# Optimization experiments

Measured on AMD Instinct MI355X. Metric: run time of the kernel, lower is better.

## Reference

```python
import jax, jax.numpy as jnp
import numpy as np

B, N, D, H = 4, 4096, 1024, 16
DH = D // H              # 64
M = int(DH * np.log(DH))  # 266 random features (performer-pytorch default)
EPS = 1e-4


def softmax_kernel(t, proj, is_query):
    # t: [B,H,N,DH], proj: [M,DH]  -> [B,H,N,M]  (FAVOR+ positive features)
    dn = t.shape[-1] ** -0.25
    ratio = proj.shape[0] ** -0.5
    td = jnp.einsum('bhnd,md->bhnm', t * dn, proj)
    diag = 0.5 * (dn ** 2) * jnp.sum(t * t, axis=-1, keepdims=True)  # [B,H,N,1]
    if is_query:
        mx = jnp.max(td, axis=-1, keepdims=True)
    else:
        mx = jnp.max(td, axis=(-1, -2), keepdims=True)
    return ratio * (jnp.exp(td - diag - mx) + EPS)


def setup_inputs() -> dict:
    key = jax.random.key(0)
    ks = jax.random.split(key, 12)
    s = 0.02
    inp = {
        'x':   jax.random.normal(ks[0], (B, N, D), jnp.float32),
        'Wq':  jax.random.normal(ks[1], (D, D), jnp.float32) * s,
        'bq':  jnp.zeros((D,), jnp.float32),
        'Wk':  jax.random.normal(ks[2], (D, D), jnp.float32) * s,
        'bk':  jnp.zeros((D,), jnp.float32),
        'Wv':  jax.random.normal(ks[3], (D, D), jnp.float32) * s,
        'bv':  jnp.zeros((D,), jnp.float32),
        'Wo':  jax.random.normal(ks[4], (D, D), jnp.float32) * s,
        'bo':  jnp.zeros((D,), jnp.float32),
        'Wfc': jax.random.normal(ks[5], (D, D), jnp.float32) * s,
        'bfc': jnp.zeros((D,), jnp.float32),
        'proj': jax.random.normal(ks[6], (M, DH), jnp.float32),  # random feature projection (frozen)
    }
    return inp


def reference(x, Wq, bq, Wk, bk, Wv, bv, Wo, bo, Wfc, bfc, proj):
    b, n, d = x.shape
    def heads(t):  # [B,N,D] -> [B,H,N,DH]
        return t.reshape(b, n, H, DH).transpose(0, 2, 1, 3)
    q = heads(x @ Wq.T + bq)
    k = heads(x @ Wk.T + bk)
    v = heads(x @ Wv.T + bv)

    qp = softmax_kernel(q, proj, is_query=True)    # [B,H,N,M]
    kp = softmax_kernel(k, proj, is_query=False)   # [B,H,N,M]

    # non-causal linear attention: O(N*M*DH)
    k_sum = jnp.sum(kp, axis=-2)                               # [B,H,M]
    d_inv = 1.0 / jnp.einsum('bhnm,bhm->bhn', qp, k_sum)       # [B,H,N]
    context = jnp.einsum('bhnm,bhnd->bhmd', kp, v)             # [B,H,M,DH]
    out = jnp.einsum('bhmd,bhnm,bhn->bhnd', context, qp, d_inv)

    out = out.transpose(0, 2, 1, 3).reshape(b, n, d)           # merge heads
    h = out @ Wo.T + bo                                        # performer internal to_out
    return jax.nn.relu(h @ Wfc.T + bfc)                        # wrapper fc_out + ReLU
```

## Files before the change

### kernel.cpp

```cpp
#include <hip/hip_runtime.h>
#include <math.h>

#define B_ 4
#define N_ 4096
#define D_ 1024
#define H_ 16
#define DH_ 64
#define M_ 266
#define MP_ 320

#define DN_ 0.35355339059327373f
#define RATIO_ 0.06131393394849658f
#define EPS_ 1e-4f
#define KP_ 72
#define NSPLIT_ 16
#define PARTSZ_ ((size_t)64 * M_ * 64)

typedef __attribute__((ext_vector_type(8))) short bfrag;
typedef __attribute__((ext_vector_type(4))) float f4;

__device__ __forceinline__ unsigned f2ord(float f) {
    unsigned u = __float_as_uint(f);
    return (u & 0x80000000u) ? ~u : (u | 0x80000000u);
}
// ... 7 lines not shown
    if (i < n) p[i] = 0.f;
}

__device__ __forceinline__ void split2pack(float x, float y, unsigned* hp, unsigned* lp) {
    unsigned ux = __float_as_uint(x), uy = __float_as_uint(y);
    float hx = __uint_as_float(ux & 0xffff0000u);
    float hy = __uint_as_float(uy & 0xffff0000u);
    float lx = x - hx, ly = y - hy;
    *hp = (ux >> 16) | (uy & 0xffff0000u);
    *lp = (__float_as_uint(lx) >> 16) | (__float_as_uint(ly) & 0xffff0000u);
}
__device__ __forceinline__ unsigned short bf16rne(float x) {
    unsigned u = __float_as_uint(x);
    return (unsigned short)((u + 0x7fffu + ((u >> 16) & 1u)) >> 16);
}

__device__ __forceinline__ void async_cp16(const void* g, void* l) {
    __builtin_amdgcn_global_load_lds(
        (const __attribute__((address_space(1))) void*)g,
        (__attribute__((address_space(3))) void*)l, 16, 0, 0);
}

__global__ __launch_bounds__(256) void split_f32(const float* __restrict__ X,
        unsigned short* __restrict__ Xh, unsigned short* __restrict__ Xl, int n4)
{
    int i = blockIdx.x * 256 + threadIdx.x;
    if (i >= n4) return;
    const float4 v = ((const float4*)X)[i];
    unsigned h0, l0, h1, l1;
    split2pack(v.x, v.y, &h0, &l0);
    split2pack(v.z, v.w, &h1, &l1);
    ((uint2*)Xh)[i] = make_uint2(h0, h1);
    ((uint2*)Xl)[i] = make_uint2(l0, l1);
}

__global__ __launch_bounds__(256) void split_w5(const float* __restrict__ W0,
        const float* __restrict__ W1, const float* __restrict__ W2,
        const float* __restrict__ W3, const float* __restrict__ W4,
        unsigned short* __restrict__ Wsp)
{
    int sel = blockIdx.y;
    const float* W = (sel == 0) ? W0 : (sel == 1) ? W1 : (sel == 2) ? W2 : (sel == 3) ? W3 : W4;
    unsigned short* h = Wsp + (size_t)sel * 2097152;
    unsigned short* l = h + 1048576;
    int i = blockIdx.x * 256 + threadIdx.x;
    const float4 v = ((const float4*)W)[i];
    unsigned h0, l0, h1, l1;
    split2pack(v.x, v.y, &h0, &l0);
    split2pack(v.z, v.w, &h1, &l1);
    ((uint2*)h)[i] = make_uint2(h0, h1);
    ((uint2*)l)[i] = make_uint2(l0, l1);
}

__global__ __launch_bounds__(256) void gemm_qkv_s(
        const unsigned short* __restrict__ Ah, const unsigned short* __restrict__ Al,
        const unsigned short* __restrict__ Wsp,
        const float* __restrict__ b0, const float* __restrict__ b1, const float* __restrict__ b2,
        float* __restrict__ C0, float* __restrict__ C1, float* __restrict__ C2)
{
    __shared__ __align__(16) unsigned short Ahs[128 * 32];
    __shared__ __align__(16) unsigned short Als[128 * 32];
    __shared__ __align__(16) unsigned short Bhs[128 * 32];
    __shared__ __align__(16) unsigned short Bls[128 * 32];

    int tid = threadIdx.x;
    int flat = blockIdx.y * 24 + blockIdx.x;
    int newid = (flat & 7) * 384 + (flat >> 3);
    int bm = (newid / 24) * 128;
    int rmod = newid % 24;
    int sel = rmod >> 3;
    int bn = (rmod & 7) * 128;
    const unsigned short* Bh = Wsp + (size_t)sel * 2097152;
    const unsigned short* Bl = Bh + 1048576;
    const float* bias = (sel == 0) ? b0 : (sel == 1) ? b1 : b2;
    float* C = (sel == 0) ? C0 : (sel == 1) ? C1 : C2;

    int lane = tid & 63;
    int w = tid >> 6;
    int wm = w >> 1, wn = w & 1;
    int ml = lane & 15, kq = lane >> 4;
    int rsub = lane >> 2;
    int ksw = (((lane & 3) ^ ((lane >> 3) & 3))) * 8;
    int slot8 = ((kq ^ ((ml >> 1) & 3))) * 8;

    f4 acc[4][4];
    #pragma unroll
    for (int i = 0; i < 4; ++i)
        #pragma unroll
        for (int j = 0; j < 4; ++j)
            acc[i][j] = (f4){0.f, 0.f, 0.f, 0.f};

    for (int kt = 0; kt < D_; kt += 32) {
        __syncthreads();
        #pragma unroll
        for (int j = 0; j < 2; ++j) {
            int row = w * 32 + j * 16;
            size_t ga = (size_t)(bm + row + rsub) * D_ + kt + ksw;
            size_t gb = (size_t)(bn + row + rsub) * D_ + kt + ksw;
            async_cp16(Ah + ga, &Ahs[row * 32]);
            async_cp16(Al + ga, &Als[row * 32]);
            async_cp16(Bh + gb, &Bhs[row * 32]);
            async_cp16(Bl + gb, &Bls[row * 32]);
        }
        __syncthreads();
        bfrag ah[4], al[4], bh[4], bl[4];
        #pragma unroll
        for (int i = 0; i < 4; ++i) {
            int arow = wm * 64 + i * 16 + ml;
            ah[i] = *(const bfrag*)&Ahs[arow * 32 + slot8];
            al[i] = *(const bfrag*)&Als[arow * 32 + slot8];
            int brow = wn * 64 + i * 16 + ml;
            bh[i] = *(const bfrag*)&Bhs[brow * 32 + slot8];
            bl[i] = *(const bfrag*)&Bls[brow * 32 + slot8];
        }
        #pragma unroll
        for (int mi = 0; mi < 4; ++mi)
            #pragma unroll
            for (int ni = 0; ni < 4; ++ni) {
                acc[mi][ni] = __builtin_amdgcn_mfma_f32_16x16x32_bf16(ah[mi], bh[ni], acc[mi][ni], 0, 0, 0);
                acc[mi][ni] = __builtin_amdgcn_mfma_f32_16x16x32_bf16(al[mi], bh[ni], acc[mi][ni], 0, 0, 0);
                acc[mi][ni] = __builtin_amdgcn_mfma_f32_16x16x32_bf16(ah[mi], bl[ni], acc[mi][ni], 0, 0, 0);
            }
    }
    #pragma unroll
    for (int ni = 0; ni < 4; ++ni) {
        int col = bn + wn * 64 + ni * 16 + ml;
        float bv = bias[col];
        #pragma unroll
        for (int mi = 0; mi < 4; ++mi) {
            int row0 = bm + wm * 64 + mi * 16 + kq * 4;
            #pragma unroll
            for (int r = 0; r < 4; ++r)
                C[(size_t)(row0 + r) * D_ + col] = acc[mi][ni][r] + bv;
        }
    }
}

__global__ __launch_bounds__(256) void gemm_nt_s(
        const unsigned short* __restrict__ Ah, const unsigned short* __restrict__ Al,
        const unsigned short* __restrict__ Bh, const unsigned short* __restrict__ Bl,
        const float* __restrict__ bias, float* __restrict__ C,
        unsigned short* __restrict__ Ch, unsigned short* __restrict__ Cl, int mode)
{
    __shared__ __align__(16) unsigned short Ahs[128 * 32];
    __shared__ __align__(16) unsigned short Als[128 * 32];
    __shared__ __align__(16) unsigned short Bhs[128 * 32];
    __shared__ __align__(16) unsigned short Bls[128 * 32];

    int tid = threadIdx.x;
    int flat = blockIdx.y * 8 + blockIdx.x;
    int newid = (flat & 7) * 128 + (flat >> 3);
    int bm = (newid >> 3) * 128;
    int bn = (newid & 7) * 128;
    int lane = tid & 63;
    int w = tid >> 6;
    int wm = w >> 1, wn = w & 1;
    int ml = lane & 15, kq = lane >> 4;
    int rsub = lane >> 2;
    int ksw = (((lane & 3) ^ ((lane >> 3) & 3))) * 8;
    int slot8 = ((kq ^ ((ml >> 1) & 3))) * 8;

    f4 acc[4][4];
    #pragma unroll
    for (int i = 0; i < 4; ++i)
        #pragma unroll
        for (int j = 0; j < 4; ++j)
            acc[i][j] = (f4){0.f, 0.f, 0.f, 0.f};

    for (int kt = 0; kt < D_; kt += 32) {
        __syncthreads();
        #pragma unroll
        for (int j = 0; j < 2; ++j) {
            int row = w * 32 + j * 16;
            size_t ga = (size_t)(bm + row + rsub) * D_ + kt + ksw;
            size_t gb = (size_t)(bn + row + rsub) * D_ + kt + ksw;
            async_cp16(Ah + ga, &Ahs[row * 32]);
            async_cp16(Al + ga, &Als[row * 32]);
            async_cp16(Bh + gb, &Bhs[row * 32]);
            async_cp16(Bl + gb, &Bls[row * 32]);
        }
        __syncthreads();
        bfrag ah[4], al[4], bh[4], bl[4];
        #pragma unroll
        for (int i = 0; i < 4; ++i) {
            int arow = wm * 64 + i * 16 + ml;
            ah[i] = *(const bfrag*)&Ahs[arow * 32 + slot8];
            al[i] = *(const bfrag*)&Als[arow * 32 + slot8];
            int brow = wn * 64 + i * 16 + ml;
            bh[i] = *(const bfrag*)&Bhs[brow * 32 + slot8];
            bl[i] = *(const bfrag*)&Bls[brow * 32 + slot8];
        }
        #pragma unroll
        for (int mi = 0; mi < 4; ++mi)
            #pragma unroll
            for (int ni = 0; ni < 4; ++ni) {
                acc[mi][ni] = __builtin_amdgcn_mfma_f32_16x16x32_bf16(ah[mi], bh[ni], acc[mi][ni], 0, 0, 0);
                acc[mi][ni] = __builtin_amdgcn_mfma_f32_16x16x32_bf16(al[mi], bh[ni], acc[mi][ni], 0, 0, 0);
                acc[mi][ni] = __builtin_amdgcn_mfma_f32_16x16x32_bf16(ah[mi], bl[ni], acc[mi][ni], 0, 0, 0);
            }
    }
    #pragma unroll
    for (int ni = 0; ni < 4; ++ni) {
        int col = bn + wn * 64 + ni * 16 + ml;
        float bv = bias[col];
        #pragma unroll
        for (int mi = 0; mi < 4; ++mi) {
            int row0 = bm + wm * 64 + mi * 16 + kq * 4;
            #pragma unroll
            for (int r = 0; r < 4; ++r) {
                float o = acc[mi][ni][r] + bv;
                size_t idx = (size_t)(row0 + r) * D_ + col;
                if (mode == 2) {
                    unsigned u = __float_as_uint(o);
                    float lo = o - __uint_as_float(u & 0xffff0000u);
                    Ch[idx] = (unsigned short)(u >> 16);
                    Cl[idx] = (unsigned short)(__float_as_uint(lo) >> 16);
                } else {
                    if (mode == 1) o = fmaxf(o, 0.f);
                    C[idx] = o;
                }
            }
        }
    }
}

__global__ __launch_bounds__(256) void kside(
    const float* __restrict__ Kin, const float* __restrict__ Vin,
    const float* __restrict__ proj,
    float* __restrict__ S_u, float* __restrict__ Cpart, float* __restrict__ C_u,
    float* __restrict__ Vsum, unsigned int* __restrict__ mxp)
{
    __shared__ __align__(16) unsigned short Kh[64 * KP_];
    __shared__ __align__(16) unsigned short VT[64 * KP_];
    __shared__ __align__(16) unsigned short Ph[2][64 * KP_];
    __shared__ __align__(16) unsigned short Us[64 * KP_];
    __shared__ __align__(16) float Ssum[MP_];
    __shared__ float diag[64];
    float* redf = (float*)Us;

    int bh = blockIdx.y, b = bh >> 4, h = bh & 15;
    int s = blockIdx.x;
    int n0 = s * 256;
    int tid = threadIdx.x, lane = tid & 63, w = tid >> 6;
    int ml = lane & 15, quad = lane >> 4;

    float* dstC = (s < NSPLIT_ - 1) ? (Cpart + (size_t)s * PARTSZ_) : C_u;

    for (int i = tid; i < MP_; i += 256) Ssum[i] = 0.f;

    f4 acc[5][4];
    #pragma unroll
    for (int i = 0; i < 5; ++i)
        #pragma unroll
        for (int j = 0; j < 4; ++j) acc[i][j] = (f4){0.f, 0.f, 0.f, 0.f};
    float vs[4] = {0.f, 0.f, 0.f, 0.f};
    float lmax = -1e30f;

    for (int nc = 0; nc < 4; ++nc) {
        __syncthreads();
        #pragma unroll
        for (int l = 0; l < 4; ++l) {
            int idx = tid + 256 * l;
            int r = idx >> 4;
            int d4 = (idx & 15) * 4;
            size_t g = ((size_t)(b * N_ + n0 + nc * 64 + r)) * D_ + h * DH_ + d4;
            const float4 kv = *(const float4*)(Kin + g);
            redf[r * 17 + (tid & 15)] = kv.x * kv.x + kv.y * kv.y + kv.z * kv.z + kv.w * kv.w;
            unsigned w0 = (unsigned)bf16rne(kv.x * DN_) | ((unsigned)bf16rne(kv.y * DN_) << 16);
            unsigned w1 = (unsigned)bf16rne(kv.z * DN_) | ((unsigned)bf16rne(kv.w * DN_) << 16);
            *(uint2*)&Kh[r * KP_ + d4] = make_uint2(w0, w1);
            const float4 vv = *(const float4*)(Vin + g);
            vs[0] += vv.x; vs[1] += vv.y; vs[2] += vv.z; vs[3] += vv.w;
            VT[(d4 + 0) * KP_ + r] = bf16rne(vv.x);
            VT[(d4 + 1) * KP_ + r] = bf16rne(vv.y);
            VT[(d4 + 2) * KP_ + r] = bf16rne(vv.z);
            VT[(d4 + 3) * KP_ + r] = bf16rne(vv.w);
        }
        {
            #pragma unroll
            for (int l = 0; l < 2; ++l) {
                int idx = tid + 256 * l;
                int m = idx >> 3, d8 = (idx & 7) * 8;
                const float4 p0 = *(const float4*)(proj + m * 64 + d8);
                const float4 p1 = *(const float4*)(proj + m * 64 + d8 + 4);
                unsigned a0 = (unsigned)bf16rne(p0.x) | ((unsigned)bf16rne(p0.y) << 16);
                unsigned a1 = (unsigned)bf16rne(p0.z) | ((unsigned)bf16rne(p0.w) << 16);
                unsigned a2 = (unsigned)bf16rne(p1.x) | ((unsigned)bf16rne(p1.y) << 16);
                unsigned a3 = (unsigned)bf16rne(p1.z) | ((unsigned)bf16rne(p1.w) << 16);
                *(uint4*)&Ph[0][m * KP_ + d8] = make_uint4(a0, a1, a2, a3);
            }
        }
        __syncthreads();
        if (tid < 64) {
            float ss = 0.f;
            #pragma unroll
            for (int p = 0; p < 16; ++p) ss += redf[tid * 17 + p];
            diag[tid] = ss * 0.0625f;
        }
        __syncthreads();

        bfrag kh0 = *(const bfrag*)&Kh[(w * 16 + ml) * KP_ + quad * 8];
        bfrag kh1 = *(const bfrag*)&Kh[(w * 16 + ml) * KP_ + 32 + quad * 8];
        float dgv[4];
        #pragma unroll
        for (int r = 0; r < 4; ++r) dgv[r] = diag[w * 16 + quad * 4 + r];

        for (int mc = 0; mc < 5; ++mc) {
            int pb = mc & 1;
            float4 pf[4];
            if (mc < 4) {
                #pragma unroll
                for (int l = 0; l < 2; ++l) {
                    int idx = tid + 256 * l;
                    int m = idx >> 3, d8 = (idx & 7) * 8;
                    int mg = (mc + 1) * 64 + m;
                    if (mg < M_) {
                        pf[l * 2 + 0] = *(const float4*)(proj + mg * 64 + d8);
                        pf[l * 2 + 1] = *(const float4*)(proj + mg * 64 + d8 + 4);
                    } else {
                        pf[l * 2 + 0] = make_float4(0.f, 0.f, 0.f, 0.f);
                        pf[l * 2 + 1] = make_float4(0.f, 0.f, 0.f, 0.f);
                    }
                }
            }
            #pragma unroll
            for (int mt = 0; mt < 4; ++mt) {
                int mrow = mt * 16 + ml;
                bfrag ph0 = *(const bfrag*)&Ph[pb][mrow * KP_ + quad * 8];
                bfrag ph1 = *(const bfrag*)&Ph[pb][mrow * KP_ + 32 + quad * 8];
                f4 t = (f4){0.f, 0.f, 0.f, 0.f};
                t = __builtin_amdgcn_mfma_f32_16x16x32_bf16(kh0, ph0, t, 0, 0, 0);
                t = __builtin_amdgcn_mfma_f32_16x16x32_bf16(kh1, ph1, t, 0, 0, 0);
                bool mv = (mc * 64 + mrow) < M_;
                float su = 0.f;
                unsigned short up[4];
                #pragma unroll
                for (int r = 0; r < 4; ++r) {
                    float u = 0.f;
                    if (mv) {
                        float tt = t[r];
                        lmax = fmaxf(lmax, tt);
                        u = __expf(tt - dgv[r]);
                    }
                    su += u;
                    up[r] = bf16rne(u);
                }
                su += __shfl_xor(su, 16);
                su += __shfl_xor(su, 32);
                if (mv && quad == 0) atomicAdd(&Ssum[mc * 64 + mrow], su);
                unsigned w0 = (unsigned)up[0] | ((unsigned)up[1] << 16);
                unsigned w1 = (unsigned)up[2] | ((unsigned)up[3] << 16);
                *(uint2*)&Us[mrow * KP_ + w * 16 + quad * 4] = make_uint2(w0, w1);
            }
            if (mc < 4) {
                #pragma unroll
                for (int l = 0; l < 2; ++l) {
                    int idx = tid + 256 * l;
                    int m = idx >> 3, d8 = (idx & 7) * 8;
                    const float4 p0 = pf[l * 2 + 0], p1 = pf[l * 2 + 1];
                    unsigned a0 = (unsigned)bf16rne(p0.x) | ((unsigned)bf16rne(p0.y) << 16);
                    unsigned a1 = (unsigned)bf16rne(p0.z) | ((unsigned)bf16rne(p0.w) << 16);
                    unsigned a2 = (unsigned)bf16rne(p1.x) | ((unsigned)bf16rne(p1.y) << 16);
                    unsigned a3 = (unsigned)bf16rne(p1.z) | ((unsigned)bf16rne(p1.w) << 16);
                    *(uint4*)&Ph[1 - pb][m * KP_ + d8] = make_uint4(a0, a1, a2, a3);
                }
            }
            __syncthreads();
            bfrag ua0 = *(const bfrag*)&Us[(w * 16 + ml) * KP_ + quad * 8];
            bfrag ua1 = *(const bfrag*)&Us[(w * 16 + ml) * KP_ + 32 + quad * 8];
            #pragma unroll
            for (int dt = 0; dt < 4; ++dt) {
                bfrag vb0 = *(const bfrag*)&VT[(dt * 16 + ml) * KP_ + quad * 8];
                bfrag vb1 = *(const bfrag*)&VT[(dt * 16 + ml) * KP_ + 32 + quad * 8];
                acc[mc][dt] = __builtin_amdgcn_mfma_f32_16x16x32_bf16(ua0, vb0, acc[mc][dt], 0, 0, 0);
                acc[mc][dt] = __builtin_amdgcn_mfma_f32_16x16x32_bf16(ua1, vb1, acc[mc][dt], 0, 0, 0);
            }
            __syncthreads();
        }
    }
    #pragma unroll
    for (int mc = 0; mc < 5; ++mc)
        #pragma unroll
        for (int dt = 0; dt < 4; ++dt)
            #pragma unroll
            for (int r = 0; r < 4; ++r) {
                int m = mc * 64 + w * 16 + quad * 4 + r;
                if (m < M_)
                    dstC[((size_t)bh * M_ + m) * 64 + dt * 16 + ml] = acc[mc][dt][r];
            }
    __syncthreads();
    for (int m = tid; m < M_; m += 256)
        atomicAdd(S_u + bh * M_ + m, Ssum[m]);
    #pragma unroll
    for (int off = 32; off; off >>= 1) lmax = fmaxf(lmax, __shfl_xor(lmax, off));
    __syncthreads();
    if (lane == 0) redf[w] = lmax;
    __syncthreads();
    if (tid == 0) {
        float mxv = fmaxf(fmaxf(redf[0], redf[1]), fmaxf(redf[2], redf[3]));
        atomicMax(mxp + bh, f2ord(mxv));
    }
    for (int j = 0; j < 4; ++j) {
        __syncthreads();
        redf[tid] = vs[j];
        __syncthreads();
        if (tid < 16) {
            float ss = 0.f;
            #pragma unroll
            for (int p = 0; p < 16; ++p) ss += redf[tid + 16 * p];
            atomicAdd(Vsum + bh * 64 + tid * 4 + j, ss);
        }
    }
}

__global__ __launch_bounds__(256) void finalize_kernel(
    const float* __restrict__ S_u, const float* __restrict__ Cpart, const float* __restrict__ C_u,
    const float* __restrict__ Vsum, const unsigned* __restrict__ mxp,
// ... 7 lines not shown
    float emx = __expf(-ord2f(mxp[bh]));

    float csacc = 0.f;
    #pragma unroll
    for (int i = 0; i < 16; ++i) {
        int idx = i * 256 + tid;
        int dh = idx & 63, mloc = idx >> 6;
        int m = mc * 64 + mloc;
        float v = 0.f;
        if (m < M_) {
            size_t off = ((size_t)bh * M_ + m) * 64 + dh;
            float sacc = C_u[off];
            for (int sp = 0; sp < NSPLIT_ - 1; ++sp)
                sacc += Cpart[(size_t)sp * PARTSZ_ + off];
            v = RATIO_ * (emx * sacc + EPS_ * Vsum[bh * 64 + dh]);
        }
        T[mloc * 65 + dh] = v;
        csacc += v;
    }
    red[tid] = csacc;
    __syncthreads();
    if (tid < 64) atomicAdd(&Cs[bh * 64 + tid], red[tid] + red[tid + 64] + red[tid + 128] + red[tid + 192]);
    float ksl = 0.f;
    if (tid < 64) {
        int m = mc * 64 + tid;
        float kv = (m < M_) ? RATIO_ * (emx * S_u[bh * M_ + m] + EPS_ * (float)N_) : 0.f;
        ksum_f[bh * MP_ + m] = kv;
        ksl = kv;
    }
    __syncthreads();
    red[tid] = ksl;
    __syncthreads();
    if (tid == 0) {
        float ss = 0.f;
        for (int p = 0; p < 64; ++p) ss += red[p];
        atomicAdd(kss + bh, ss);
    }
    __syncthreads();
    #pragma unroll
    for (int i = 0; i < 8; ++i) {
        int idx = i * 256 + tid;
        int dh = idx >> 5, m2 = (idx & 31) * 2;
        float v0 = T[m2 * 65 + dh], v1 = T[(m2 + 1) * 65 + dh];
        unsigned u0 = __float_as_uint(v0), u1 = __float_as_uint(v1);
        float lo0 = v0 - __uint_as_float(u0 & 0xffff0000u);
        float lo1 = v1 - __uint_as_float(u1 & 0xffff0000u);
        size_t dst = ((size_t)(bh * 64 + dh)) * MP_ + mc * 64 + m2;
        *(unsigned*)&ctxTh[dst] = (u0 >> 16) | (u1 & 0xffff0000u);
        *(unsigned*)&ctxTl[dst] = (__float_as_uint(lo0) >> 16) | (__float_as_uint(lo1) & 0xffff0000u);
    }
}

__global__ __launch_bounds__(256) void qattn(
    const float* __restrict__ Q, const float* __restrict__ proj,
    const float* __restrict__ ksum_f, const unsigned short* __restrict__ ctxTh,
    const unsigned short* __restrict__ ctxTl,
    const float* __restrict__ Cs, const float* __restrict__ kss,
    unsigned short* __restrict__ attnH, unsigned short* __restrict__ attnL)
{
    __shared__ __align__(16) unsigned short Qh[64 * KP_], Ql[64 * KP_];
    __shared__ __align__(16) unsigned short Ph[64 * KP_], Pl[64 * KP_];
    __shared__ __align__(16) unsigned short Uh[64 * KP_], Ul[64 * KP_];
    __shared__ __align__(16) float ks[MP_];
    __shared__ float diag[64];
    float* redf = (float*)Uh;

    int bh = blockIdx.y, b = bh >> 4, h = bh & 15;
    int n0 = blockIdx.x * 64;
    int tid = threadIdx.x, lane = tid & 63, w = tid >> 6;
    int ml = lane & 15, quad = lane >> 4;

    #pragma unroll
    for (int l = 0; l < 4; ++l) {
        int idx = tid + 256 * l;
        int r = idx >> 4, d4 = (idx & 15) * 4;
        size_t g = ((size_t)(b * N_ + n0 + r)) * D_ + h * DH_ + d4;
        const float4 qv = *(const float4*)(Q + g);
        redf[r * 17 + (tid & 15)] = qv.x * qv.x + qv.y * qv.y + qv.z * qv.z + qv.w * qv.w;
        unsigned h0, l0, h1, l1;
        split2pack(qv.x * DN_, qv.y * DN_, &h0, &l0);
        split2pack(qv.z * DN_, qv.w * DN_, &h1, &l1);
        *(uint2*)&Qh[r * KP_ + d4] = make_uint2(h0, h1);
        *(uint2*)&Ql[r * KP_ + d4] = make_uint2(l0, l1);
    }
    for (int m = tid; m < MP_; m += 256) ks[m] = ksum_f[bh * MP_ + m];
    __syncthreads();
    if (tid < 64) {
        float s = 0.f;
        #pragma unroll
        for (int p = 0; p < 16; ++p) s += redf[tid * 17 + p];
        diag[tid] = s * 0.0625f;
    }
    __syncthreads();

    bfrag qh0 = *(const bfrag*)&Qh[(w * 16 + ml) * KP_ + quad * 8];
    bfrag ql0 = *(const bfrag*)&Ql[(w * 16 + ml) * KP_ + quad * 8];
    bfrag qh1 = *(const bfrag*)&Qh[(w * 16 + ml) * KP_ + 32 + quad * 8];
    bfrag ql1 = *(const bfrag*)&Ql[(w * 16 + ml) * KP_ + 32 + quad * 8];
    float dg = diag[w * 16 + ml];
    float dacc = 0.f, tmax = -1e30f;
    f4 oacc[4];
    #pragma unroll
    for (int i = 0; i < 4; ++i) oacc[i] = (f4){0.f, 0.f, 0.f, 0.f};

    for (int mc = 0; mc < 5; ++mc) {
        #pragma unroll
        for (int l = 0; l < 4; ++l) {
            int idx = tid + 256 * l;
            int m = idx >> 4, d4 = (idx & 15) * 4;
            int mg = mc * 64 + m;
            float4 p = make_float4(0.f, 0.f, 0.f, 0.f);
            if (mg < M_) p = *(const float4*)(proj + mg * 64 + d4);
            unsigned h0, l0, h1, l1;
            split2pack(p.x, p.y, &h0, &l0);
            split2pack(p.z, p.w, &h1, &l1);
            *(uint2*)&Ph[m * KP_ + d4] = make_uint2(h0, h1);
            *(uint2*)&Pl[m * KP_ + d4] = make_uint2(l0, l1);
        }
        __syncthreads();
        #pragma unroll
        for (int mt = 0; mt < 4; ++mt) {
            int mrow = mt * 16 + ml;
            bfrag ph0 = *(const bfrag*)&Ph[mrow * KP_ + quad * 8];
            bfrag pl0 = *(const bfrag*)&Pl[mrow * KP_ + quad * 8];
            bfrag ph1 = *(const bfrag*)&Ph[mrow * KP_ + 32 + quad * 8];
            bfrag pl1 = *(const bfrag*)&Pl[mrow * KP_ + 32 + quad * 8];
            f4 t = (f4){0.f, 0.f, 0.f, 0.f};
            t = __builtin_amdgcn_mfma_f32_16x16x32_bf16(ph0, qh0, t, 0, 0, 0);
            t = __builtin_amdgcn_mfma_f32_16x16x32_bf16(pl0, qh0, t, 0, 0, 0);
            t = __builtin_amdgcn_mfma_f32_16x16x32_bf16(ph0, ql0, t, 0, 0, 0);
            t = __builtin_amdgcn_mfma_f32_16x16x32_bf16(ph1, qh1, t, 0, 0, 0);
            t = __builtin_amdgcn_mfma_f32_16x16x32_bf16(pl1, qh1, t, 0, 0, 0);
            t = __builtin_amdgcn_mfma_f32_16x16x32_bf16(ph1, ql1, t, 0, 0, 0);
            const float4 ksv = *(const float4*)&ks[mc * 64 + mt * 16 + quad * 4];
            float ksa[4] = {ksv.x, ksv.y, ksv.z, ksv.w};
            unsigned short uh4[4], ul4[4];
            #pragma unroll
            for (int r = 0; r < 4; ++r) {
                int mg = mc * 64 + mt * 16 + quad * 4 + r;
                float tt = t[r];
                float u = __expf(tt - dg);
                if (mg < M_) tmax = fmaxf(tmax, tt);
                dacc = fmaf(u, ksa[r], dacc);
                unsigned uu = __float_as_uint(u);
                float lo = u - __uint_as_float(uu & 0xffff0000u);
                uh4[r] = (unsigned short)(uu >> 16);
                ul4[r] = (unsigned short)(__float_as_uint(lo) >> 16);
            }
            unsigned a0 = (unsigned)uh4[0] | ((unsigned)uh4[1] << 16);
            unsigned a1 = (unsigned)uh4[2] | ((unsigned)uh4[3] << 16);
            unsigned b0 = (unsigned)ul4[0] | ((unsigned)ul4[1] << 16);
            unsigned b1 = (unsigned)ul4[2] | ((unsigned)ul4[3] << 16);
            *(uint2*)&Uh[(w * 16 + ml) * KP_ + mt * 16 + quad * 4] = make_uint2(a0, a1);
            *(uint2*)&Ul[(w * 16 + ml) * KP_ + mt * 16 + quad * 4] = make_uint2(b0, b1);
        }
        __syncthreads();
        #pragma unroll
        for (int l = 0; l < 2; ++l) {
            int idx = tid + 256 * l;
            int dh = idx >> 3, m8 = (idx & 7) * 8;
            size_t src = ((size_t)(bh * 64 + dh)) * MP_ + mc * 64 + m8;
            *(uint4*)&Ph[dh * KP_ + m8] = *(const uint4*)(ctxTh + src);
            *(uint4*)&Pl[dh * KP_ + m8] = *(const uint4*)(ctxTl + src);
        }
        __syncthreads();
        bfrag ua0h = *(const bfrag*)&Uh[(w * 16 + ml) * KP_ + quad * 8];
        bfrag ua0l = *(const bfrag*)&Ul[(w * 16 + ml) * KP_ + quad * 8];
        bfrag ua1h = *(const bfrag*)&Uh[(w * 16 + ml) * KP_ + 32 + quad * 8];
        bfrag ua1l = *(const bfrag*)&Ul[(w * 16 + ml) * KP_ + 32 + quad * 8];
        #pragma unroll
// ... 25 lines not shown
            float dv = __shfl(dinv, srcl);
            float fv = __shfl(fac, srcl);
            float o = (oacc[dt][r] + fv * csv) * dv;
            int n = n0 + w * 16 + quad * 4 + r;
            size_t gi = ((size_t)(b * N_ + n)) * D_ + h * DH_ + dt * 16 + ml;
            unsigned u = __float_as_uint(o);
            float lo = o - __uint_as_float(u & 0xffff0000u);
            attnH[gi] = (unsigned short)(u >> 16);
            attnL[gi] = (unsigned short)(__float_as_uint(lo) >> 16);
        }
    }
}

extern "C" void kernel_launch(void* const* d_in, const int* in_sizes, int n_in,
                              void* d_out, int out_size, void* d_ws, size_t ws_size,
                              hipStream_t stream)
{
    const float* x    = (const float*)d_in[0];
    const float* Wq   = (const float*)d_in[1];
    const float* bq   = (const float*)d_in[2];
    const float* Wk   = (const float*)d_in[3];
    const float* bk   = (const float*)d_in[4];
    const float* Wv   = (const float*)d_in[5];
    const float* bv   = (const float*)d_in[6];
    const float* Wo   = (const float*)d_in[7];
    const float* bo   = (const float*)d_in[8];
    const float* Wfc  = (const float*)d_in[9];
    const float* bfc  = (const float*)d_in[10];
    const float* proj = (const float*)d_in[11];
    float* out = (float*)d_out;

    float* ws = (float*)d_ws;
    const size_t nTok = (size_t)B_ * N_ * D_;
    const size_t nSu  = 64 * M_;
    const size_t nCu  = (size_t)64 * M_ * 64;
    const size_t nVs  = 64 * 64;
    const size_t nMx  = 64;
    const size_t nKsf = 64 * MP_;
    const size_t nCtx = (size_t)64 * MP_ * 64;
    const size_t nCs  = 64 * 64;

    const size_t offQ   = 0;
    const size_t offK   = nTok;
    const size_t offV   = nTok * 2;
    const size_t offSu  = nTok * 3;
    const size_t offCu  = offSu + nSu;
    const size_t offVs  = offCu + nCu;
    const size_t offMx  = offVs + nVs;
    const size_t offKsf = offMx + nMx;
    const size_t offCtx = offKsf + nKsf;
    const size_t offCs  = offCtx + nCtx;
    const size_t offKss = offCs + nCs;
    const size_t offWsp = offKss + 64;

    float* Q    = ws + offQ;
    float* Kb   = ws + offK;
    float* Vb   = ws + offV;
    float* S_u  = ws + offSu;
    float* C_u  = ws + offCu;
    float* Vsum = ws + offVs;
    unsigned* mx = (unsigned*)(ws + offMx);
    float* ksf  = ws + offKsf;
    unsigned short* ctxTh = (unsigned short*)(ws + offCtx);
    unsigned short* ctxTl = ctxTh + (size_t)64 * 64 * MP_;
    float* Cs   = ws + offCs;
    float* kss  = ws + offKss;
    unsigned short* Wsp = (unsigned short*)(ws + offWsp);

    unsigned short* xh = (unsigned short*)out;
    unsigned short* xl = xh + nTok;
    unsigned short* attnH = (unsigned short*)Kb;
    unsigned short* attnL = attnH + nTok;
    unsigned short* hbH = (unsigned short*)Vb;
    unsigned short* hbL = hbH + nTok;
    float* Cpart = out;

    int nzero = (int)(nSu + nCu + nVs + nMx + nKsf + nCtx + nCs + 64);
    zero_kernel<<<dim3((nzero + 255) / 256), dim3(256), 0, stream>>>(S_u, nzero);

    split_f32<<<dim3(16384), dim3(256), 0, stream>>>(x, xh, xl, (int)(nTok / 4));
    split_w5<<<dim3(1024, 5), dim3(256), 0, stream>>>(Wq, Wk, Wv, Wo, Wfc, Wsp);

    gemm_qkv_s<<<dim3(24, (B_ * N_) / 128), dim3(256), 0, stream>>>(
        xh, xl, Wsp, bq, bk, bv, Q, Kb, Vb);

    kside<<<dim3(NSPLIT_, 64), dim3(256), 0, stream>>>(Kb, Vb, proj, S_u, Cpart, C_u, Vsum, mx);
    finalize_kernel<<<dim3(5, 64), dim3(256), 0, stream>>>(S_u, Cpart, C_u, Vsum, mx, ksf, ctxTh, ctxTl, Cs, kss);
    qattn<<<dim3(64, 64), dim3(256), 0, stream>>>(Q, proj, ksf, ctxTh, ctxTl, Cs, kss, attnH, attnL);

    dim3 gg(D_ / 128, (B_ * N_) / 128);
    gemm_nt_s<<<gg, dim3(256), 0, stream>>>(attnH, attnL,
        Wsp + (size_t)3 * 2097152, Wsp + (size_t)3 * 2097152 + 1048576,
        bo, (float*)nullptr, hbH, hbL, 2);
    gemm_nt_s<<<gg, dim3(256), 0, stream>>>(hbH, hbL,
        Wsp + (size_t)4 * 2097152, Wsp + (size_t)4 * 2097152 + 1048576,
        bfc, out, (unsigned short*)nullptr, (unsigned short*)nullptr, 1);
}
```

Measured before the change: 988.7 us.

## Double-buffer LDS tiles in split-bf16 GEMMs and drop block swizzle

Both GEMM kernels now use two shared-memory buffers per operand and prefetch the next K tile while computing the current one, with one barrier per iteration instead of two. The intent is to overlap global-to-LDS async copies with MFMA work. The XCD-aware block-index remapping is removed in favour of plain grid indexing. Shared memory per block doubles to 64 KB, which can lower occupancy. The async copies have no explicit wait before the barrier, so it is unclear whether the prefetched data is guaranteed visible before it is read.

```diff
diff --git a/kernel.cpp b/kernel.cpp
--- a/kernel.cpp
+++ b/kernel.cpp
@@ -89,18 +89,15 @@
         const float* __restrict__ b0, const float* __restrict__ b1, const float* __restrict__ b2,
         float* __restrict__ C0, float* __restrict__ C1, float* __restrict__ C2)
 {
-    __shared__ __align__(16) unsigned short Ahs[128 * 32];
-    __shared__ __align__(16) unsigned short Als[128 * 32];
-    __shared__ __align__(16) unsigned short Bhs[128 * 32];
-    __shared__ __align__(16) unsigned short Bls[128 * 32];
+    __shared__ __align__(16) unsigned short Ahs[2][128 * 32];
+    __shared__ __align__(16) unsigned short Als[2][128 * 32];
+    __shared__ __align__(16) unsigned short Bhs[2][128 * 32];
+    __shared__ __align__(16) unsigned short Bls[2][128 * 32];
 
     int tid = threadIdx.x;
-    int flat = blockIdx.y * 24 + blockIdx.x;
-    int newid = (flat & 7) * 384 + (flat >> 3);
-    int bm = (newid / 24) * 128;
-    int rmod = newid % 24;
-    int sel = rmod >> 3;
-    int bn = (rmod & 7) * 128;
+    int sel = blockIdx.x >> 3;
+    int bn = (blockIdx.x & 7) * 128;
+    int bm = blockIdx.y * 128;
     const unsigned short* Bh = Wsp + (size_t)sel * 2097152;
     const unsigned short* Bl = Bh + 1048576;
     const float* bias = (sel == 0) ? b0 : (sel == 1) ? b1 : b2;
@@ -121,28 +118,34 @@
         for (int j = 0; j < 4; ++j)
             acc[i][j] = (f4){0.f, 0.f, 0.f, 0.f};
 
-    for (int kt = 0; kt < D_; kt += 32) {
-        __syncthreads();
+    auto STAGE = [&](int kt, int pb) {
         #pragma unroll
         for (int j = 0; j < 2; ++j) {
             int row = w * 32 + j * 16;
             size_t ga = (size_t)(bm + row + rsub) * D_ + kt + ksw;
             size_t gb = (size_t)(bn + row + rsub) * D_ + kt + ksw;
-            async_cp16(Ah + ga, &Ahs[row * 32]);
-            async_cp16(Al + ga, &Als[row * 32]);
-            async_cp16(Bh + gb, &Bhs[row * 32]);
-            async_cp16(Bl + gb, &Bls[row * 32]);
-        }
-        __syncthreads();
+            async_cp16(Ah + ga, &Ahs[pb][row * 32]);
+            async_cp16(Al + ga, &Als[pb][row * 32]);
+            async_cp16(Bh + gb, &Bhs[pb][row * 32]);
+            async_cp16(Bl + gb, &Bls[pb][row * 32]);
+        }
+    };
+
+    STAGE(0, 0);
+    __syncthreads();
+
+    for (int t = 0; t < 32; ++t) {
+        int pb = t & 1;
+        if (t < 31) STAGE((t + 1) * 32, pb ^ 1);
         bfrag ah[4], al[4], bh[4], bl[4];
         #pragma unroll
         for (int i = 0; i < 4; ++i) {
             int arow = wm * 64 + i * 16 + ml;
-            ah[i] = *(const bfrag*)&Ahs[arow * 32 + slot8];
-            al[i] = *(const bfrag*)&Als[arow * 32 + slot8];
+            ah[i] = *(const bfrag*)&Ahs[pb][arow * 32 + slot8];
+            al[i] = *(const bfrag*)&Als[pb][arow * 32 + slot8];
             int brow = wn * 64 + i * 16 + ml;
-            bh[i] = *(const bfrag*)&Bhs[brow * 32 + slot8];
-            bl[i] = *(const bfrag*)&Bls[brow * 32 + slot8];
+            bh[i] = *(const bfrag*)&Bhs[pb][brow * 32 + slot8];
+            bl[i] = *(const bfrag*)&Bls[pb][brow * 32 + slot8];
         }
         #pragma unroll
         for (int mi = 0; mi < 4; ++mi)
@@ -152,6 +155,7 @@
                 acc[mi][ni] = __builtin_amdgcn_mfma_f32_16x16x32_bf16(al[mi], bh[ni], acc[mi][ni], 0, 0, 0);
                 acc[mi][ni] = __builtin_amdgcn_mfma_f32_16x16x32_bf16(ah[mi], bl[ni], acc[mi][ni], 0, 0, 0);
             }
+        __syncthreads();
     }
     #pragma unroll
     for (int ni = 0; ni < 4; ++ni) {
@@ -173,16 +177,14 @@
         const float* __restrict__ bias, float* __restrict__ C,
         unsigned short* __restrict__ Ch, unsigned short* __restrict__ Cl, int mode)
 {
-    __shared__ __align__(16) unsigned short Ahs[128 * 32];
-    __shared__ __align__(16) unsigned short Als[128 * 32];
-    __shared__ __align__(16) unsigned short Bhs[128 * 32];
-    __shared__ __align__(16) unsigned short Bls[128 * 32];
+    __shared__ __align__(16) unsigned short Ahs[2][128 * 32];
+    __shared__ __align__(16) unsigned short Als[2][128 * 32];
+    __shared__ __align__(16) unsigned short Bhs[2][128 * 32];
+    __shared__ __align__(16) unsigned short Bls[2][128 * 32];
 
     int tid = threadIdx.x;
-    int flat = blockIdx.y * 8 + blockIdx.x;
-    int newid = (flat & 7) * 128 + (flat >> 3);
-    int bm = (newid >> 3) * 128;
-    int bn = (newid & 7) * 128;
+    int bn = blockIdx.x * 128;
+    int bm = blockIdx.y * 128;
     int lane = tid & 63;
     int w = tid >> 6;
     int wm = w >> 1, wn = w & 1;
@@ -198,28 +200,34 @@
         for (int j = 0; j < 4; ++j)
             acc[i][j] = (f4){0.f, 0.f, 0.f, 0.f};
 
-    for (int kt = 0; kt < D_; kt += 32) {
-        __syncthreads();
+    auto STAGE = [&](int kt, int pb) {
         #pragma unroll
         for (int j = 0; j < 2; ++j) {
             int row = w * 32 + j * 16;
             size_t ga = (size_t)(bm + row + rsub) * D_ + kt + ksw;
             size_t gb = (size_t)(bn + row + rsub) * D_ + kt + ksw;
-            async_cp16(Ah + ga, &Ahs[row * 32]);
-            async_cp16(Al + ga, &Als[row * 32]);
-            async_cp16(Bh + gb, &Bhs[row * 32]);
-            async_cp16(Bl + gb, &Bls[row * 32]);
-        }
-        __syncthreads();
+            async_cp16(Ah + ga, &Ahs[pb][row * 32]);
+            async_cp16(Al + ga, &Als[pb][row * 32]);
+            async_cp16(Bh + gb, &Bhs[pb][row * 32]);
+            async_cp16(Bl + gb, &Bls[pb][row * 32]);
+        }
+    };
+
+    STAGE(0, 0);
+    __syncthreads();
+
+    for (int t = 0; t < 32; ++t) {
+        int pb = t & 1;
+        if (t < 31) STAGE((t + 1) * 32, pb ^ 1);
         bfrag ah[4], al[4], bh[4], bl[4];
         #pragma unroll
         for (int i = 0; i < 4; ++i) {
             int arow = wm * 64 + i * 16 + ml;
-            ah[i] = *(const bfrag*)&Ahs[arow * 32 + slot8];
-            al[i] = *(const bfrag*)&Als[arow * 32 + slot8];
+            ah[i] = *(const bfrag*)&Ahs[pb][arow * 32 + slot8];
+            al[i] = *(const bfrag*)&Als[pb][arow * 32 + slot8];
             int brow = wn * 64 + i * 16 + ml;
-            bh[i] = *(const bfrag*)&Bhs[brow * 32 + slot8];
-            bl[i] = *(const bfrag*)&Bls[brow * 32 + slot8];
+            bh[i] = *(const bfrag*)&Bhs[pb][brow * 32 + slot8];
+            bl[i] = *(const bfrag*)&Bls[pb][brow * 32 + slot8];
         }
         #pragma unroll
         for (int mi = 0; mi < 4; ++mi)
@@ -229,6 +237,7 @@
                 acc[mi][ni] = __builtin_amdgcn_mfma_f32_16x16x32_bf16(al[mi], bh[ni], acc[mi][ni], 0, 0, 0);
                 acc[mi][ni] = __builtin_amdgcn_mfma_f32_16x16x32_bf16(ah[mi], bl[ni], acc[mi][ni], 0, 0, 0);
             }
+        __syncthreads();
     }
     #pragma unroll
     for (int ni = 0; ni < 4; ++ni) {
```

After: 1.100 ms. 1.11x slower.

## Enlarge split-bf16 GEMM tiles to 256x256 with 512-thread blocks

Applied to the files above, without the earlier changes.

The QKV and the two output-projection GEMMs now use 256x256 output tiles computed by 8 waves in 512-thread blocks, up from 128x128 tiles with 4 waves. Each wave owns a 128x64 sub-tile and loads its A fragments one row-block at a time inside the MFMA loop. The goal is to roughly halve global and LDS traffic per output element and raise MFMA work per barrier. In exchange the kernels need 64KB of LDS per block and about 128 accumulator registers per thread, and the block-id swizzle used for L2 locality is removed. The smaller grids also risk poor load balance, since the output-projection GEMMs now launch only 256 blocks.

```diff
diff --git a/kernel.cpp b/kernel.cpp
--- a/kernel.cpp
+++ b/kernel.cpp
@@ -83,24 +83,21 @@
     ((uint2*)l)[i] = make_uint2(l0, l1);
 }
 
-__global__ __launch_bounds__(256) void gemm_qkv_s(
+__global__ __launch_bounds__(512) void gemm_qkv_s(
         const unsigned short* __restrict__ Ah, const unsigned short* __restrict__ Al,
         const unsigned short* __restrict__ Wsp,
         const float* __restrict__ b0, const float* __restrict__ b1, const float* __restrict__ b2,
         float* __restrict__ C0, float* __restrict__ C1, float* __restrict__ C2)
 {
-    __shared__ __align__(16) unsigned short Ahs[128 * 32];
-    __shared__ __align__(16) unsigned short Als[128 * 32];
-    __shared__ __align__(16) unsigned short Bhs[128 * 32];
-    __shared__ __align__(16) unsigned short Bls[128 * 32];
+    __shared__ __align__(16) unsigned short Ahs[256 * 32];
+    __shared__ __align__(16) unsigned short Als[256 * 32];
+    __shared__ __align__(16) unsigned short Bhs[256 * 32];
+    __shared__ __align__(16) unsigned short Bls[256 * 32];
 
     int tid = threadIdx.x;
-    int flat = blockIdx.y * 24 + blockIdx.x;
-    int newid = (flat & 7) * 384 + (flat >> 3);
-    int bm = (newid / 24) * 128;
-    int rmod = newid % 24;
-    int sel = rmod >> 3;
-    int bn = (rmod & 7) * 128;
+    int sel = blockIdx.x >> 2;
+    int bn = (blockIdx.x & 3) * 256;
+    int bm = blockIdx.y * 256;
     const unsigned short* Bh = Wsp + (size_t)sel * 2097152;
     const unsigned short* Bl = Bh + 1048576;
     const float* bias = (sel == 0) ? b0 : (sel == 1) ? b1 : b2;
@@ -108,15 +105,15 @@
 
     int lane = tid & 63;
     int w = tid >> 6;
-    int wm = w >> 1, wn = w & 1;
+    int wm = w >> 2, wn = w & 3;
     int ml = lane & 15, kq = lane >> 4;
     int rsub = lane >> 2;
     int ksw = (((lane & 3) ^ ((lane >> 3) & 3))) * 8;
     int slot8 = ((kq ^ ((ml >> 1) & 3))) * 8;
 
-    f4 acc[4][4];
-    #pragma unroll
-    for (int i = 0; i < 4; ++i)
+    f4 acc[8][4];
+    #pragma unroll
+    for (int i = 0; i < 8; ++i)
         #pragma unroll
         for (int j = 0; j < 4; ++j)
             acc[i][j] = (f4){0.f, 0.f, 0.f, 0.f};
@@ -134,32 +131,33 @@
             async_cp16(Bl + gb, &Bls[row * 32]);
         }
         __syncthreads();
-        bfrag ah[4], al[4], bh[4], bl[4];
-        #pragma unroll
-        for (int i = 0; i < 4; ++i) {
-            int arow = wm * 64 + i * 16 + ml;
-            ah[i] = *(const bfrag*)&Ahs[arow * 32 + slot8];
-            al[i] = *(const bfrag*)&Als[arow * 32 + slot8];
-            int brow = wn * 64 + i * 16 + ml;
-            bh[i] = *(const bfrag*)&Bhs[brow * 32 + slot8];
-            bl[i] = *(const bfrag*)&Bls[brow * 32 + slot8];
-        }
-        #pragma unroll
-        for (int mi = 0; mi < 4; ++mi)
+        bfrag bh[4], bl[4];
+        #pragma unroll
+        for (int ni = 0; ni < 4; ++ni) {
+            int brow = wn * 64 + ni * 16 + ml;
+            bh[ni] = *(const bfrag*)&Bhs[brow * 32 + slot8];
+            bl[ni] = *(const bfrag*)&Bls[brow * 32 + slot8];
+        }
+        #pragma unroll
+        for (int mi = 0; mi < 8; ++mi) {
+            int arow = wm * 128 + mi * 16 + ml;
+            bfrag ah = *(const bfrag*)&Ahs[arow * 32 + slot8];
+            bfrag al = *(const bfrag*)&Als[arow * 32 + slot8];
             #pragma unroll
             for (int ni = 0; ni < 4; ++ni) {
-                acc[mi][ni] = __builtin_amdgcn_mfma_f32_16x16x32_bf16(ah[mi], bh[ni], acc[mi][ni], 0, 0, 0);
-                acc[mi][ni] = __builtin_amdgcn_mfma_f32_16x16x32_bf16(al[mi], bh[ni], acc[mi][ni], 0, 0, 0);
-                acc[mi][ni] = __builtin_amdgcn_mfma_f32_16x16x32_bf16(ah[mi], bl[ni], acc[mi][ni], 0, 0, 0);
-            }
+                acc[mi][ni] = __builtin_amdgcn_mfma_f32_16x16x32_bf16(ah, bh[ni], acc[mi][ni], 0, 0, 0);
+                acc[mi][ni] = __builtin_amdgcn_mfma_f32_16x16x32_bf16(al, bh[ni], acc[mi][ni], 0, 0, 0);
+                acc[mi][ni] = __builtin_amdgcn_mfma_f32_16x16x32_bf16(ah, bl[ni], acc[mi][ni], 0, 0, 0);
+            }
+        }
     }
     #pragma unroll
     for (int ni = 0; ni < 4; ++ni) {
         int col = bn + wn * 64 + ni * 16 + ml;
         float bv = bias[col];
         #pragma unroll
-        for (int mi = 0; mi < 4; ++mi) {
-            int row0 = bm + wm * 64 + mi * 16 + kq * 4;
+        for (int mi = 0; mi < 8; ++mi) {
+            int row0 = bm + wm * 128 + mi * 16 + kq * 4;
             #pragma unroll
             for (int r = 0; r < 4; ++r)
                 C[(size_t)(row0 + r) * D_ + col] = acc[mi][ni][r] + bv;
@@ -167,33 +165,31 @@
     }
 }
 
-__global__ __launch_bounds__(256) void gemm_nt_s(
+__global__ __launch_bounds__(512) void gemm_nt_s(
         const unsigned short* __restrict__ Ah, const unsigned short* __restrict__ Al,
         const unsigned short* __restrict__ Bh, const unsigned short* __restrict__ Bl,
         const float* __restrict__ bias, float* __restrict__ C,
         unsigned short* __restrict__ Ch, unsigned short* __restrict__ Cl, int mode)
 {
-    __shared__ __align__(16) unsigned short Ahs[128 * 32];
-    __shared__ __align__(16) unsigned short Als[128 * 32];
-    __shared__ __align__(16) unsigned short Bhs[128 * 32];
-    __shared__ __align__(16) unsigned short Bls[128 * 32];
+    __shared__ __align__(16) unsigned short Ahs[256 * 32];
+    __shared__ __align__(16) unsigned short Als[256 * 32];
+    __shared__ __align__(16) unsigned short Bhs[256 * 32];
+    __shared__ __align__(16) unsigned short Bls[256 * 32];
 
     int tid = threadIdx.x;
-    int flat = blockIdx.y * 8 + blockIdx.x;
-    int newid = (flat & 7) * 128 + (flat >> 3);
-    int bm = (newid >> 3) * 128;
-    int bn = (newid & 7) * 128;
+    int bn = blockIdx.x * 256;
+    int bm = blockIdx.y * 256;
     int lane = tid & 63;
     int w = tid >> 6;
-    int wm = w >> 1, wn = w & 1;
+    int wm = w >> 2, wn = w & 3;
     int ml = lane & 15, kq = lane >> 4;
     int rsub = lane >> 2;
     int ksw = (((lane & 3) ^ ((lane >> 3) & 3))) * 8;
     int slot8 = ((kq ^ ((ml >> 1) & 3))) * 8;
 
-    f4 acc[4][4];
-    #pragma unroll
-    for (int i = 0; i < 4; ++i)
+    f4 acc[8][4];
+    #pragma unroll
+    for (int i = 0; i < 8; ++i)
         #pragma unroll
         for (int j = 0; j < 4; ++j)
             acc[i][j] = (f4){0.f, 0.f, 0.f, 0.f};
@@ -211,32 +207,33 @@
             async_cp16(Bl + gb, &Bls[row * 32]);
         }
         __syncthreads();
-        bfrag ah[4], al[4], bh[4], bl[4];
-        #pragma unroll
-        for (int i = 0; i < 4; ++i) {
-            int arow = wm * 64 + i * 16 + ml;
-            ah[i] = *(const bfrag*)&Ahs[arow * 32 + slot8];
-            al[i] = *(const bfrag*)&Als[arow * 32 + slot8];
-            int brow = wn * 64 + i * 16 + ml;
-            bh[i] = *(const bfrag*)&Bhs[brow * 32 + slot8];
-            bl[i] = *(const bfrag*)&Bls[brow * 32 + slot8];
-        }
-        #pragma unroll
-        for (int mi = 0; mi < 4; ++mi)
+        bfrag bh[4], bl[4];
+        #pragma unroll
+        for (int ni = 0; ni < 4; ++ni) {
+            int brow = wn * 64 + ni * 16 + ml;
+            bh[ni] = *(const bfrag*)&Bhs[brow * 32 + slot8];
+            bl[ni] = *(const bfrag*)&Bls[brow * 32 + slot8];
+        }
+        #pragma unroll
+        for (int mi = 0; mi < 8; ++mi) {
+            int arow = wm * 128 + mi * 16 + ml;
+            bfrag ah = *(const bfrag*)&Ahs[arow * 32 + slot8];
+            bfrag al = *(const bfrag*)&Als[arow * 32 + slot8];
             #pragma unroll
             for (int ni = 0; ni < 4; ++ni) {
-                acc[mi][ni] = __builtin_amdgcn_mfma_f32_16x16x32_bf16(ah[mi], bh[ni], acc[mi][ni], 0, 0, 0);
-                acc[mi][ni] = __builtin_amdgcn_mfma_f32_16x16x32_bf16(al[mi], bh[ni], acc[mi][ni], 0, 0, 0);
-                acc[mi][ni] = __builtin_amdgcn_mfma_f32_16x16x32_bf16(ah[mi], bl[ni], acc[mi][ni], 0, 0, 0);
-            }
+                acc[mi][ni] = __builtin_amdgcn_mfma_f32_16x16x32_bf16(ah, bh[ni], acc[mi][ni], 0, 0, 0);
+                acc[mi][ni] = __builtin_amdgcn_mfma_f32_16x16x32_bf16(al, bh[ni], acc[mi][ni], 0, 0, 0);
+                acc[mi][ni] = __builtin_amdgcn_mfma_f32_16x16x32_bf16(ah, bl[ni], acc[mi][ni], 0, 0, 0);
+            }
+        }
     }
     #pragma unroll
     for (int ni = 0; ni < 4; ++ni) {
         int col = bn + wn * 64 + ni * 16 + ml;
         float bv = bias[col];
         #pragma unroll
-        for (int mi = 0; mi < 4; ++mi) {
-            int row0 = bm + wm * 64 + mi * 16 + kq * 4;
+        for (int mi = 0; mi < 8; ++mi) {
+            int row0 = bm + wm * 128 + mi * 16 + kq * 4;
             #pragma unroll
             for (int r = 0; r < 4; ++r) {
                 float o = acc[mi][ni][r] + bv;
@@ -731,18 +728,18 @@
     split_f32<<<dim3(16384), dim3(256), 0, stream>>>(x, xh, xl, (int)(nTok / 4));
     split_w5<<<dim3(1024, 5), dim3(256), 0, stream>>>(Wq, Wk, Wv, Wo, Wfc, Wsp);
 
-    gemm_qkv_s<<<dim3(24, (B_ * N_) / 128), dim3(256), 0, stream>>>(
+    gemm_qkv_s<<<dim3(12, (B_ * N_) / 256), dim3(512), 0, stream>>>(
         xh, xl, Wsp, bq, bk, bv, Q, Kb, Vb);
 
     kside<<<dim3(NSPLIT_, 64), dim3(256), 0, stream>>>(Kb, Vb, proj, S_u, Cpart, C_u, Vsum, mx);
     finalize_kernel<<<dim3(5, 64), dim3(256), 0, stream>>>(S_u, Cpart, C_u, Vsum, mx, ksf, ctxTh, ctxTl, Cs, kss);
     qattn<<<dim3(64, 64), dim3(256), 0, stream>>>(Q, proj, ksf, ctxTh, ctxTl, Cs, kss, attnH, attnL);
 
-    dim3 gg(D_ / 128, (B_ * N_) / 128);
-    gemm_nt_s<<<gg, dim3(256), 0, stream>>>(attnH, attnL,
+    dim3 gg(D_ / 256, (B_ * N_) / 256);
+    gemm_nt_s<<<gg, dim3(512), 0, stream>>>(attnH, attnL,
         Wsp + (size_t)3 * 2097152, Wsp + (size_t)3 * 2097152 + 1048576,
         bo, (float*)nullptr, hbH, hbL, 2);
-    gemm_nt_s<<<gg, dim3(256), 0, stream>>>(hbH, hbL,
+    gemm_nt_s<<<gg, dim3(512), 0, stream>>>(hbH, hbL,
         Wsp + (size_t)4 * 2097152, Wsp + (size_t)4 * 2097152 + 1048576,
         bfc, out, (unsigned short*)nullptr, (unsigned short*)nullptr, 1);
 }
```

Result: slower. 1.009 ms (+2.0%).

## Presplit projection matrix once and drop XCD-aware block remapping in GEMMs

Applied to the files above, without the earlier changes.

Adds a small kernel that converts the random-feature projection into bf16 (rounded) and hi/lo split bf16 buffers once, zero-padded to 320 rows. kside and qattn then copy these ready-made bf16 rows into shared memory instead of loading fp32 and converting inside every block. Separately, the block-index swizzle that grouped tiles across XCDs in both GEMM kernels is replaced by plain row-major tile mapping. Removing the swizzle may hurt L2 locality on the multi-XCD device, which could offset the savings in the attention kernels.

```diff
diff --git a/kernel.cpp b/kernel.cpp
--- a/kernel.cpp
+++ b/kernel.cpp
@@ -83,6 +83,20 @@
     ((uint2*)l)[i] = make_uint2(l0, l1);
 }
 
+__global__ __launch_bounds__(256) void presplit_proj(const float* __restrict__ proj,
+        unsigned short* __restrict__ projR, unsigned short* __restrict__ projHg,
+        unsigned short* __restrict__ projLg)
+{
+    int i = blockIdx.x * 256 + threadIdx.x;
+    int m = i >> 6, d = i & 63;
+    float v = (m < M_) ? proj[m * 64 + d] : 0.f;
+    projR[i] = bf16rne(v);
+    unsigned u = __float_as_uint(v);
+    float lo = v - __uint_as_float(u & 0xffff0000u);
+    projHg[i] = (unsigned short)(u >> 16);
+    projLg[i] = (unsigned short)(__float_as_uint(lo) >> 16);
+}
+
 __global__ __launch_bounds__(256) void gemm_qkv_s(
         const unsigned short* __restrict__ Ah, const unsigned short* __restrict__ Al,
         const unsigned short* __restrict__ Wsp,
@@ -95,12 +109,9 @@
     __shared__ __align__(16) unsigned short Bls[128 * 32];
 
     int tid = threadIdx.x;
-    int flat = blockIdx.y * 24 + blockIdx.x;
-    int newid = (flat & 7) * 384 + (flat >> 3);
-    int bm = (newid / 24) * 128;
-    int rmod = newid % 24;
-    int sel = rmod >> 3;
-    int bn = (rmod & 7) * 128;
+    int sel = blockIdx.x >> 3;
+    int bn = (blockIdx.x & 7) * 128;
+    int bm = blockIdx.y * 128;
     const unsigned short* Bh = Wsp + (size_t)sel * 2097152;
     const unsigned short* Bl = Bh + 1048576;
     const float* bias = (sel == 0) ? b0 : (sel == 1) ? b1 : b2;
@@ -179,10 +190,8 @@
     __shared__ __align__(16) unsigned short Bls[128 * 32];
 
     int tid = threadIdx.x;
-    int flat = blockIdx.y * 8 + blockIdx.x;
-    int newid = (flat & 7) * 128 + (flat >> 3);
-    int bm = (newid >> 3) * 128;
-    int bn = (newid & 7) * 128;
+    int bn = blockIdx.x * 128;
+    int bm = blockIdx.y * 128;
     int lane = tid & 63;
     int w = tid >> 6;
     int wm = w >> 1, wn = w & 1;
@@ -257,7 +266,7 @@
 
 __global__ __launch_bounds__(256) void kside(
     const float* __restrict__ Kin, const float* __restrict__ Vin,
-    const float* __restrict__ proj,
+    const unsigned short* __restrict__ projR,
     float* __restrict__ S_u, float* __restrict__ Cpart, float* __restrict__ C_u,
     float* __restrict__ Vsum, unsigned int* __restrict__ mxp)
 {
@@ -312,13 +321,7 @@
             for (int l = 0; l < 2; ++l) {
                 int idx = tid + 256 * l;
                 int m = idx >> 3, d8 = (idx & 7) * 8;
-                const float4 p0 = *(const float4*)(proj + m * 64 + d8);
-                const float4 p1 = *(const float4*)(proj + m * 64 + d8 + 4);
-                unsigned a0 = (unsigned)bf16rne(p0.x) | ((unsigned)bf16rne(p0.y) << 16);
-                unsigned a1 = (unsigned)bf16rne(p0.z) | ((unsigned)bf16rne(p0.w) << 16);
-                unsigned a2 = (unsigned)bf16rne(p1.x) | ((unsigned)bf16rne(p1.y) << 16);
-                unsigned a3 = (unsigned)bf16rne(p1.z) | ((unsigned)bf16rne(p1.w) << 16);
-                *(uint4*)&Ph[0][m * KP_ + d8] = make_uint4(a0, a1, a2, a3);
+                *(uint4*)&Ph[0][m * KP_ + d8] = *(const uint4*)(projR + m * 64 + d8);
             }
         }
         __syncthreads();
@@ -338,20 +341,14 @@
 
         for (int mc = 0; mc < 5; ++mc) {
             int pb = mc & 1;
-            float4 pf[4];
+            uint4 pf2[2];
             if (mc < 4) {
                 #pragma unroll
                 for (int l = 0; l < 2; ++l) {
                     int idx = tid + 256 * l;
                     int m = idx >> 3, d8 = (idx & 7) * 8;
                     int mg = (mc + 1) * 64 + m;
-                    if (mg < M_) {
-                        pf[l * 2 + 0] = *(const float4*)(proj + mg * 64 + d8);
-                        pf[l * 2 + 1] = *(const float4*)(proj + mg * 64 + d8 + 4);
-                    } else {
-                        pf[l * 2 + 0] = make_float4(0.f, 0.f, 0.f, 0.f);
-                        pf[l * 2 + 1] = make_float4(0.f, 0.f, 0.f, 0.f);
-                    }
+                    pf2[l] = *(const uint4*)(projR + mg * 64 + d8);
                 }
             }
             #pragma unroll
@@ -388,12 +385,7 @@
                 for (int l = 0; l < 2; ++l) {
                     int idx = tid + 256 * l;
                     int m = idx >> 3, d8 = (idx & 7) * 8;
-                    const float4 p0 = pf[l * 2 + 0], p1 = pf[l * 2 + 1];
-                    unsigned a0 = (unsigned)bf16rne(p0.x) | ((unsigned)bf16rne(p0.y) << 16);
-                    unsigned a1 = (unsigned)bf16rne(p0.z) | ((unsigned)bf16rne(p0.w) << 16);
-                    unsigned a2 = (unsigned)bf16rne(p1.x) | ((unsigned)bf16rne(p1.y) << 16);
-                    unsigned a3 = (unsigned)bf16rne(p1.z) | ((unsigned)bf16rne(p1.w) << 16);
-                    *(uint4*)&Ph[1 - pb][m * KP_ + d8] = make_uint4(a0, a1, a2, a3);
+                    *(uint4*)&Ph[1 - pb][m * KP_ + d8] = pf2[l];
                 }
             }
             __syncthreads();
@@ -507,7 +499,8 @@
 }
 
 __global__ __launch_bounds__(256) void qattn(
-    const float* __restrict__ Q, const float* __restrict__ proj,
+    const float* __restrict__ Q, const unsigned short* __restrict__ projHg,
+    const unsigned short* __restrict__ projLg,
     const float* __restrict__ ksum_f, const unsigned short* __restrict__ ctxTh,
     const unsigned short* __restrict__ ctxTl,
     const float* __restrict__ Cs, const float* __restrict__ kss,
@@ -560,17 +553,12 @@
 
     for (int mc = 0; mc < 5; ++mc) {
         #pragma unroll
-        for (int l = 0; l < 4; ++l) {
+        for (int l = 0; l < 2; ++l) {
             int idx = tid + 256 * l;
-            int m = idx >> 4, d4 = (idx & 15) * 4;
+            int m = idx >> 3, d8 = (idx & 7) * 8;
             int mg = mc * 64 + m;
-            float4 p = make_float4(0.f, 0.f, 0.f, 0.f);
-            if (mg < M_) p = *(const float4*)(proj + mg * 64 + d4);
-            unsigned h0, l0, h1, l1;
-            split2pack(p.x, p.y, &h0, &l0);
-            split2pack(p.z, p.w, &h1, &l1);
-            *(uint2*)&Ph[m * KP_ + d4] = make_uint2(h0, h1);
-            *(uint2*)&Pl[m * KP_ + d4] = make_uint2(l0, l1);
+            *(uint4*)&Ph[m * KP_ + d8] = *(const uint4*)(projHg + mg * 64 + d8);
+            *(uint4*)&Pl[m * KP_ + d8] = *(const uint4*)(projLg + mg * 64 + d8);
         }
         __syncthreads();
         #pragma unroll
@@ -702,6 +690,7 @@
     const size_t offCs  = offCtx + nCtx;
     const size_t offKss = offCs + nCs;
     const size_t offWsp = offKss + 64;
+    const size_t offPrj = offWsp + 5242880;
 
     float* Q    = ws + offQ;
     float* Kb   = ws + offK;
@@ -716,6 +705,9 @@
     float* Cs   = ws + offCs;
     float* kss  = ws + offKss;
     unsigned short* Wsp = (unsigned short*)(ws + offWsp);
+    unsigned short* projR  = (unsigned short*)(ws + offPrj);
+    unsigned short* projHg = projR + (size_t)MP_ * 64;
+    unsigned short* projLg = projHg + (size_t)MP_ * 64;
 
     unsigned short* xh = (unsigned short*)out;
     unsigned short* xl = xh + nTok;
@@ -730,13 +722,14 @@
 
     split_f32<<<dim3(16384), dim3(256), 0, stream>>>(x, xh, xl, (int)(nTok / 4));
     split_w5<<<dim3(1024, 5), dim3(256), 0, stream>>>(Wq, Wk, Wv, Wo, Wfc, Wsp);
+    presplit_proj<<<dim3(80), dim3(256), 0, stream>>>(proj, projR, projHg, projLg);
 
     gemm_qkv_s<<<dim3(24, (B_ * N_) / 128), dim3(256), 0, stream>>>(
         xh, xl, Wsp, bq, bk, bv, Q, Kb, Vb);
 
-    kside<<<dim3(NSPLIT_, 64), dim3(256), 0, stream>>>(Kb, Vb, proj, S_u, Cpart, C_u, Vsum, mx);
+    kside<<<dim3(NSPLIT_, 64), dim3(256), 0, stream>>>(Kb, Vb, projR, S_u, Cpart, C_u, Vsum, mx);
     finalize_kernel<<<dim3(5, 64), dim3(256), 0, stream>>>(S_u, Cpart, C_u, Vsum, mx, ksf, ctxTh, ctxTl, Cs, kss);
-    qattn<<<dim3(64, 64), dim3(256), 0, stream>>>(Q, proj, ksf, ctxTh, ctxTl, Cs, kss, attnH, attnL);
+    qattn<<<dim3(64, 64), dim3(256), 0, stream>>>(Q, projHg, projLg, ksf, ctxTh, ctxTl, Cs, kss, attnH, attnL);
 
     dim3 gg(D_ / 128, (B_ * N_) / 128);
     gemm_nt_s<<<gg, dim3(256), 0, stream>>>(attnH, attnL,
```

After: 988.1 us. About the same (-0.1%).
